# Kernel optimization log

Measured on AMD Instinct MI355X. Metric: run time of the kernel, lower is better.

## Reference

```python
import jax, jax.numpy as jnp
import numpy as np
from jax import lax

TEMP = 0.05
MOMENTUM = 0.9
EPS = 1e-12


def _l2_normalize(x, axis=-1):
    n = jnp.sqrt(jnp.sum(x * x, axis=axis, keepdims=True))
    return x / jnp.maximum(n, EPS)


def _cross_entropy(logits, targets):
    # mean over batch of -log_softmax(logits)[target]
    logp = jax.nn.log_softmax(logits, axis=-1)
    return -jnp.mean(jnp.take_along_axis(logp, targets[:, None], axis=-1))


def _momentum_update(features, x, targets, m):
    # Sequential per-sample read-modify-write (faithful to the torch loop,
    # matters when targets contain duplicates). carry = memory bank.
    def step(f, xy):
        x_i, y_i = xy
        row = m * f[y_i] + (1.0 - m) * x_i
        row = row / jnp.linalg.norm(row)
        return f.at[y_i].set(row), None
    f, _ = lax.scan(step, features, (x, targets))
    return f


def setup_inputs() -> dict:
    key = jax.random.key(0)
    k1, k2, k3, k4, k5, k6 = jax.random.split(key, 6)
    B, D, N = 512, 1024, 16384
    inputs_rgb = jax.random.normal(k1, (B, D), dtype=jnp.float32)
    inputs_ir = jax.random.normal(k2, (B, D), dtype=jnp.float32)
    targets_rgb = jax.random.randint(k3, (B,), 0, N, dtype=jnp.int32)
    targets_ir = jax.random.randint(k4, (B,), 0, N, dtype=jnp.int32)
    # memory banks (buffers); initialized as normalized random rows to mimic a
    # warmed-up cluster memory (the module starts at zeros, degenerate for CE)
    features_rgb = _l2_normalize(jax.random.normal(k5, (N, D), dtype=jnp.float32))
    features_ir = _l2_normalize(jax.random.normal(k6, (N, D), dtype=jnp.float32))
    return {"inputs_rgb": inputs_rgb, "inputs_ir": inputs_ir,
            "targets_rgb": targets_rgb, "targets_ir": targets_ir,
            "features_rgb": features_rgb, "features_ir": features_ir}


def reference(inputs_rgb, inputs_ir, targets_rgb, targets_ir, features_rgb, features_ir):
    x_rgb = _l2_normalize(inputs_rgb)  # [B, D]
    x_ir = _l2_normalize(inputs_ir)
    logits_rgb = (x_rgb @ features_rgb.T) / TEMP  # [B, N]
    logits_ir = (x_ir @ features_ir.T) / TEMP
    loss_rgb = _cross_entropy(logits_rgb, targets_rgb)
    loss_ir = _cross_entropy(logits_ir, targets_ir)
    # side-effect of CM.backward in the original: momentum scatter update + renorm
    # (change_scale == 1.0 so the Hungarian cross-modal exchange is skipped)
    new_features_rgb = _momentum_update(features_rgb, x_rgb, targets_rgb, MOMENTUM)
    new_features_ir = _momentum_update(features_ir, x_ir, targets_ir, MOMENTUM)
    return (loss_rgb, loss_ir, new_features_rgb, new_features_ir)
```

## Files before the change

### kernel.cpp

```cpp
#include <hip/hip_runtime.h>
#include <math.h>

#define BATCH 512
#define DIM   1024
#define NCLUS 16384
#define TINV  20.0f

typedef __attribute__((ext_vector_type(4))) float f32x4;
typedef __attribute__((ext_vector_type(2))) float f32x2;
typedef __attribute__((ext_vector_type(8))) short bf16x8;

static __device__ __forceinline__ unsigned short f2bf(float f) {
  unsigned int u = __float_as_uint(f);
  u += 0x7FFFu + ((u >> 16) & 1u);
  return (unsigned short)(u >> 16);
}

typedef const __attribute__((address_space(1))) unsigned int* gas1_t;
typedef __attribute__((address_space(3))) unsigned int* las3_t;
static __device__ __forceinline__ void gload16(const void* g, void* l) {
  __builtin_amdgcn_global_load_lds((gas1_t)g, (las3_t)l, 16, 0, 0);
}

__global__ void nrm_kernel(const float* __restrict__ in_rgb,
                           const float* __restrict__ in_ir,
                           float* __restrict__ xf,
                           unsigned short* __restrict__ xb,
                           float* __restrict__ accum) {
  int gid = blockIdx.x * blockDim.x + threadIdx.x;
  if (gid < 2048) accum[gid] = 0.0f;

  int row = blockIdx.x;
  int mod = row >> 9;
  int r   = row & 511;
  const float* in = (mod ? in_ir : in_rgb) + (size_t)r * DIM;
  float* xo          = xf + ((size_t)mod * BATCH + r) * DIM;
  unsigned short* xbo = xb + ((size_t)mod * BATCH + r) * DIM;

  int t = threadIdx.x;
  float4 v = ((const float4*)in)[t];
  float ss = v.x*v.x + v.y*v.y + v.z*v.z + v.w*v.w;
#pragma unroll
  for (int m = 1; m < 64; m <<= 1) ss += __shfl_xor(ss, m, 64);
  __shared__ float red[4];
  if ((t & 63) == 0) red[t >> 6] = ss;
  __syncthreads();
  float inv = 1.0f / fmaxf(sqrtf(red[0] + red[1] + red[2] + red[3]), 1e-12f);
  float4 o = make_float4(v.x * inv, v.y * inv, v.z * inv, v.w * inv);
  ((float4*)xo)[t] = o;
  ushort4 ob = make_ushort4(f2bf(o.x), f2bf(o.y), f2bf(o.z), f2bf(o.w));
  ((ushort4*)xbo)[t] = ob;
}

__global__ void cvtcopy_kernel(const float* __restrict__ f_rgb,
                               const float* __restrict__ f_ir,
                               float* __restrict__ out,
                               unsigned short* __restrict__ fb) {
  const size_t n4 = (size_t)NCLUS * DIM / 4;
  size_t stride = (size_t)gridDim.x * blockDim.x;
  for (size_t i = (size_t)blockIdx.x * blockDim.x + threadIdx.x; i < 2 * n4; i += stride) {
    const f32x4* src = (i < n4) ? ((const f32x4*)f_rgb) + i
                                : ((const f32x4*)f_ir) + (i - n4);
    const f32x4 v = __builtin_nontemporal_load(src);
    f32x2* o2 = (f32x2*)(out + 4 * i);
    __builtin_nontemporal_store((f32x2){v.x, v.y}, o2);
    __builtin_nontemporal_store((f32x2){v.z, v.w}, o2 + 1);
    ((ushort4*)fb)[i] = make_ushort4(f2bf(v.x), f2bf(v.y), f2bf(v.z), f2bf(v.w));
  }
}

#define BM 256
#define BN 256
#define BK 32
#define KT_N (DIM / BK)

__launch_bounds__(512, 2)
__global__ void gemm_lse_kernel(const unsigned short* __restrict__ xb,
                                const unsigned short* __restrict__ fb,
                                const int* __restrict__ t_rgb,
                                const int* __restrict__ t_ir,
                                float* __restrict__ rowsum,
                                float* __restrict__ tgtlog) {
  const int nt  = blockIdx.x;
  const int bt  = blockIdx.y & 1;
  const int mod = blockIdx.y >> 1;

  const unsigned short* X = xb + ((size_t)mod * BATCH + bt * BM) * DIM;
  const unsigned short* F = fb + ((size_t)mod * NCLUS + (size_t)nt * BN) * DIM;
  const int* tg = mod ? t_ir : t_rgb;
  float* rs = rowsum + mod * BATCH;
  float* tl = tgtlog + mod * BATCH;

  __shared__ __align__(16) unsigned short Ab[4][BM * BK];
  __shared__ __align__(16) unsigned short Bb[4][BN * BK];

  const int tid  = threadIdx.x;
  const int wid  = tid >> 6;
  const int lane = tid & 63;
  const int wr = wid >> 2, wc = wid & 3;
  const int l15 = lane & 15, lhi = lane >> 4;
  const int sw = (l15 & 6) << 3;

  f32x4 acc[8][4];
#pragma unroll
  for (int m = 0; m < 8; ++m)
#pragma unroll
    for (int n = 0; n < 4; ++n) acc[m][n] = (f32x4){0.f, 0.f, 0.f, 0.f};

  auto STAGE_A = [&](int sl, int kt) {
#pragma unroll
    for (int c = 0; c < 2; ++c) {
      int q = c * 512 + tid;
      int cs = (q & 3) ^ ((q >> 3) & 3);
      gload16(X + (size_t)(q >> 2) * DIM + kt * BK + cs * 8,
              &Ab[sl][(c * 512 + wid * 64) * 8]);
    }
  };
  auto STAGE_B = [&](int sl, int kt) {
#pragma unroll
    for (int c = 0; c < 2; ++c) {
      int q = c * 512 + tid;
      int cs = (q & 3) ^ ((q >> 3) & 3);
      gload16(F + (size_t)(q >> 2) * DIM + kt * BK + cs * 8,
              &Bb[sl][(c * 512 + wid * 64) * 8]);
    }
  };
  auto LDA = [&](int sl, int row) {
    return *(const bf16x8*)((const char*)Ab[sl] + ((row * (BK * 2) + lhi * 16) ^ sw));
  };
  auto LDB = [&](int sl, int row) {
    return *(const bf16x8*)((const char*)Bb[sl] + ((row * (BK * 2) + lhi * 16) ^ sw));
  };

  auto ITERATION = [&](int i, bool doStage, int gate) {
    const int sl = i & 3, sp = (i + 2) & 3;
    bf16x8 a[8], b[4];
#pragma unroll
    for (int n = 0; n < 4; ++n) b[n] = LDB(sl, wc * 64 + n * 16 + l15);
#pragma unroll
    for (int m = 0; m < 8; ++m) a[m] = LDA(sl, wr * 128 + m * 16 + l15);
    if (doStage) { STAGE_A(sp, i + 2); STAGE_B(sp, i + 2); }
    __builtin_amdgcn_s_setprio(1);
#pragma unroll
    for (int m = 0; m < 8; ++m)
#pragma unroll
      for (int n = 0; n < 4; ++n)
        acc[m][n] = __builtin_amdgcn_mfma_f32_16x16x32_bf16(a[m], b[n], acc[m][n], 0, 0, 0);
    __builtin_amdgcn_s_setprio(0);
    if (gate >= 0) {
      if (gate == 4) asm volatile("s_waitcnt vmcnt(4)" ::: "memory");
      else           asm volatile("s_waitcnt vmcnt(0)" ::: "memory");
      __builtin_amdgcn_s_barrier();
    }
  };

  STAGE_A(0, 0); STAGE_B(0, 0);
  STAGE_A(1, 1); STAGE_B(1, 1);
  asm volatile("s_waitcnt vmcnt(4)" ::: "memory");
  __builtin_amdgcn_s_barrier();

  for (int i = 0; i < KT_N - 2; ++i) ITERATION(i, true, 4);
  ITERATION(KT_N - 2, false, 0);
  ITERATION(KT_N - 1, false, -1);

#pragma unroll
  for (int M = 0; M < 8; ++M) {
    const int browbase = bt * BM + wr * 128 + ((M >> 2) << 6) + ((M & 3) << 4) + (lhi << 2);
    float esum[4];
#pragma unroll
    for (int j = 0; j < 4; ++j) {
      const int brow = browbase + j;
      const int t = tg[brow];
      float e = 0.f;
#pragma unroll
      for (int n = 0; n < 4; ++n) {
        float logit = acc[M][n][j] * TINV;
        e += __expf(logit);
        int col = nt * BN + wc * 64 + n * 16 + l15;
        if (col == t) tl[brow] = logit;
      }
      esum[j] = e;
    }
#pragma unroll
    for (int j = 0; j < 4; ++j) {
      float e = esum[j];
      e += __shfl_xor(e, 1, 64);
      e += __shfl_xor(e, 2, 64);
      e += __shfl_xor(e, 4, 64);
      e += __shfl_xor(e, 8, 64);
      if (l15 == 0) atomicAdd(rs + browbase + j, e);
    }
  }
}

__global__ void loss_kernel(const float* __restrict__ rowsum,
                            const float* __restrict__ tgtlog,
                            float* __restrict__ out) {
  int t = threadIdx.x;
  float lr = logf(rowsum[t]) - tgtlog[t];
  float li = logf(rowsum[BATCH + t]) - tgtlog[BATCH + t];
#pragma unroll
  for (int m = 1; m < 64; m <<= 1) { lr += __shfl_xor(lr, m, 64); li += __shfl_xor(li, m, 64); }
  __shared__ float sr[8], si[8];
  if ((t & 63) == 0) { sr[t >> 6] = lr; si[t >> 6] = li; }
  __syncthreads();
  if (t == 0) {
    float a = 0.f, b = 0.f;
#pragma unroll
    for (int i = 0; i < 8; ++i) { a += sr[i]; b += si[i]; }
    out[0] = a * (1.0f / BATCH);
    out[1] = b * (1.0f / BATCH);
  }
}

__global__ void mom_kernel(const int* __restrict__ t_rgb,
                           const int* __restrict__ t_ir,
                           const float* __restrict__ xf,
                           float* __restrict__ out) {
  const int i   = blockIdx.x;
  const int mod = blockIdx.y;
  const int* tg = mod ? t_ir : t_rgb;
  const int y = tg[i];
  for (int j = 0; j < i; ++j)
    if (tg[j] == y) return;

  const float* x = xf + (size_t)mod * BATCH * DIM;
  float* rowp = out + (size_t)mod * NCLUS * DIM + (size_t)y * DIM;

  const int t = threadIdx.x;
  float2 r0 = ((const float2*)rowp)[t];
  float2 r1 = ((const float2*)rowp)[t + 256];
  __shared__ float red[4];

  for (int j = i; j < BATCH; ++j) {
    if (tg[j] != y) continue;
    const float2* xr = (const float2*)(x + (size_t)j * DIM);
    float2 x0 = xr[t], x1 = xr[t + 256];
    r0.x = 0.9f * r0.x + 0.1f * x0.x;
    r0.y = 0.9f * r0.y + 0.1f * x0.y;
    r1.x = 0.9f * r1.x + 0.1f * x1.x;
    r1.y = 0.9f * r1.y + 0.1f * x1.y;
    float ss = r0.x*r0.x + r0.y*r0.y + r1.x*r1.x + r1.y*r1.y;
#pragma unroll
    for (int m = 1; m < 64; m <<= 1) ss += __shfl_xor(ss, m, 64);
    if ((t & 63) == 0) red[t >> 6] = ss;
    __syncthreads();
    float tot = red[0] + red[1] + red[2] + red[3];
    __syncthreads();
    float inv = 1.0f / sqrtf(tot);
    r0.x *= inv; r0.y *= inv; r1.x *= inv; r1.y *= inv;
  }
  ((float2*)rowp)[t] = r0;
  ((float2*)rowp)[t + 256] = r1;
}

extern "C" void kernel_launch(void* const* d_in, const int* in_sizes, int n_in,
                              void* d_out, int out_size, void* d_ws, size_t ws_size,
                              hipStream_t stream) {
  (void)in_sizes; (void)n_in; (void)out_size; (void)ws_size;
  const float* in_rgb = (const float*)d_in[0];
  const float* in_ir  = (const float*)d_in[1];
  const int*   t_rgb  = (const int*)d_in[2];
  const int*   t_ir   = (const int*)d_in[3];
  const float* f_rgb  = (const float*)d_in[4];
  const float* f_ir   = (const float*)d_in[5];
  float* out = (float*)d_out;

  char* ws = (char*)d_ws;
  float*          xf     = (float*)ws;
  unsigned short* xb     = (unsigned short*)(ws + (4u<<20));
  float*          rowsum = (float*)(ws + (6u<<20));
  float*          tgtlog = rowsum + 1024;
  unsigned short* fb     = (unsigned short*)(ws + (8u<<20));

  nrm_kernel<<<1024, 256, 0, stream>>>(in_rgb, in_ir, xf, xb, rowsum);
  cvtcopy_kernel<<<8192, 256, 0, stream>>>(f_rgb, f_ir, out + 2, fb);
  gemm_lse_kernel<<<dim3(64, 4), 512, 0, stream>>>(xb, fb, t_rgb, t_ir, rowsum, tgtlog);
  mom_kernel<<<dim3(512, 2), 256, 0, stream>>>(t_rgb, t_ir, xf, out + 2);
  loss_kernel<<<1, 512, 0, stream>>>(rowsum, tgtlog, out);
}
```

Measured before the change: 184.7 us.

## Replace four-slot LDS prefetch pipeline with simple double buffering

Measured after the change: 192.4 us. 1.04x slower.

```diff
diff --git a/kernel.cpp b/kernel.cpp
--- a/kernel.cpp
+++ b/kernel.cpp
@@ -91,8 +91,8 @@
   float* rs = rowsum + mod * BATCH;
   float* tl = tgtlog + mod * BATCH;
 
-  __shared__ __align__(16) unsigned short Ab[4][BM * BK];
-  __shared__ __align__(16) unsigned short Bb[4][BN * BK];
+  __shared__ __align__(16) unsigned short Ab[2][BM * BK];
+  __shared__ __align__(16) unsigned short Bb[2][BN * BK];
 
   const int tid  = threadIdx.x;
   const int wid  = tid >> 6;
@@ -107,61 +107,52 @@
 #pragma unroll
     for (int n = 0; n < 4; ++n) acc[m][n] = (f32x4){0.f, 0.f, 0.f, 0.f};
 
-  auto STAGE_A = [&](int sl, int kt) {
+  auto STAGE_A = [&](int buf, int kt) {
 #pragma unroll
     for (int c = 0; c < 2; ++c) {
       int q = c * 512 + tid;
       int cs = (q & 3) ^ ((q >> 3) & 3);
       gload16(X + (size_t)(q >> 2) * DIM + kt * BK + cs * 8,
-              &Ab[sl][(c * 512 + wid * 64) * 8]);
-    }
-  };
-  auto STAGE_B = [&](int sl, int kt) {
+              &Ab[buf][(c * 512 + wid * 64) * 8]);
+    }
+  };
+  auto STAGE_B = [&](int buf, int kt) {
 #pragma unroll
     for (int c = 0; c < 2; ++c) {
       int q = c * 512 + tid;
       int cs = (q & 3) ^ ((q >> 3) & 3);
       gload16(F + (size_t)(q >> 2) * DIM + kt * BK + cs * 8,
-              &Bb[sl][(c * 512 + wid * 64) * 8]);
-    }
-  };
-  auto LDA = [&](int sl, int row) {
-    return *(const bf16x8*)((const char*)Ab[sl] + ((row * (BK * 2) + lhi * 16) ^ sw));
-  };
-  auto LDB = [&](int sl, int row) {
-    return *(const bf16x8*)((const char*)Bb[sl] + ((row * (BK * 2) + lhi * 16) ^ sw));
-  };
-
-  auto ITERATION = [&](int i, bool doStage, int gate) {
-    const int sl = i & 3, sp = (i + 2) & 3;
+              &Bb[buf][(c * 512 + wid * 64) * 8]);
+    }
+  };
+  auto LDA = [&](int buf, int row) {
+    return *(const bf16x8*)((const char*)Ab[buf] + ((row * (BK * 2) + lhi * 16) ^ sw));
+  };
+  auto LDB = [&](int buf, int row) {
+    return *(const bf16x8*)((const char*)Bb[buf] + ((row * (BK * 2) + lhi * 16) ^ sw));
+  };
+
+  STAGE_A(0, 0); STAGE_B(0, 0);
+  __syncthreads();
+
+  for (int s = 0; s < KT_N; ++s) {
+    const int cur = s & 1;
+    if (s + 1 < KT_N) {
+      STAGE_A(cur ^ 1, s + 1);
+      STAGE_B(cur ^ 1, s + 1);
+    }
     bf16x8 a[8], b[4];
 #pragma unroll
-    for (int n = 0; n < 4; ++n) b[n] = LDB(sl, wc * 64 + n * 16 + l15);
-#pragma unroll
-    for (int m = 0; m < 8; ++m) a[m] = LDA(sl, wr * 128 + m * 16 + l15);
-    if (doStage) { STAGE_A(sp, i + 2); STAGE_B(sp, i + 2); }
-    __builtin_amdgcn_s_setprio(1);
+    for (int n = 0; n < 4; ++n) b[n] = LDB(cur, wc * 64 + n * 16 + l15);
+#pragma unroll
+    for (int m = 0; m < 8; ++m) a[m] = LDA(cur, wr * 128 + m * 16 + l15);
 #pragma unroll
     for (int m = 0; m < 8; ++m)
 #pragma unroll
       for (int n = 0; n < 4; ++n)
         acc[m][n] = __builtin_amdgcn_mfma_f32_16x16x32_bf16(a[m], b[n], acc[m][n], 0, 0, 0);
-    __builtin_amdgcn_s_setprio(0);
-    if (gate >= 0) {
-      if (gate == 4) asm volatile("s_waitcnt vmcnt(4)" ::: "memory");
-      else           asm volatile("s_waitcnt vmcnt(0)" ::: "memory");
-      __builtin_amdgcn_s_barrier();
-    }
-  };
-
-  STAGE_A(0, 0); STAGE_B(0, 0);
-  STAGE_A(1, 1); STAGE_B(1, 1);
-  asm volatile("s_waitcnt vmcnt(4)" ::: "memory");
-  __builtin_amdgcn_s_barrier();
-
-  for (int i = 0; i < KT_N - 2; ++i) ITERATION(i, true, 4);
-  ITERATION(KT_N - 2, false, 0);
-  ITERATION(KT_N - 1, false, -1);
+    __syncthreads();
+  }
 
 #pragma unroll
   for (int M = 0; M < 8; ++M) {
```
